# Optimization experiments

Hardware: AMD Instinct MI355X
Metric: run time of the kernel (lower is better)

Reference implementation:

```python
import jax, jax.numpy as jnp
import numpy as np

N_USERS = 100000
N_ITEMS = 20000
N_GENRES = 20
N_TAGS = 1128
EMB_ID = 64
EMB_FEAT = 64
HEADS = 8
HIDDEN = 256
D_MOVIE = EMB_ID + 2 * EMB_FEAT  # 192
E_HALF = 200000
N_NODES = N_USERS + N_ITEMS
NEG_SLOPE = 0.2


def setup_inputs() -> dict:
    key = jax.random.key(0)
    ks = jax.random.split(key, 24)
    p = lambda k, shape: (jax.random.normal(k, shape, jnp.float32) * 0.05)
    user_ids = jnp.arange(N_USERS)
    movie_ids = jnp.arange(N_ITEMS)
    mov_x = jax.random.normal(ks[0], (N_ITEMS, N_GENRES + N_TAGS), jnp.float32)
    # bipartite user<->movie edges, both directions (no self loops, matches add_self_loops=False)
    u = jax.random.randint(ks[1], (E_HALF,), 0, N_USERS)
    m = jax.random.randint(ks[2], (E_HALF,), 0, N_ITEMS) + N_USERS
    edge_index = jnp.stack([jnp.concatenate([u, m]), jnp.concatenate([m, u])])  # [2, 2*E_HALF]
    C1 = HIDDEN // HEADS
    return dict(
        user_ids=user_ids, movie_ids=movie_ids, mov_x=mov_x, edge_index=edge_index,
        user_emb=p(ks[3], (N_USERS, EMB_ID)), item_emb=p(ks[4], (N_ITEMS, EMB_ID)),
        gW1=p(ks[5], (N_GENRES, EMB_FEAT)), gb1=jnp.zeros((EMB_FEAT,), jnp.float32),
        gW2=p(ks[6], (EMB_FEAT, EMB_FEAT)), gb2=jnp.zeros((EMB_FEAT,), jnp.float32),
        tW1=p(ks[7], (N_TAGS, EMB_FEAT)), tb1=jnp.zeros((EMB_FEAT,), jnp.float32),
        tW2=p(ks[8], (EMB_FEAT, EMB_FEAT)), tb2=jnp.zeros((EMB_FEAT,), jnp.float32),
        Ws1=p(ks[9], (D_MOVIE, HIDDEN)), Wd1=p(ks[10], (D_MOVIE, HIDDEN)),
        as1=p(ks[11], (HEADS, C1)), ad1=p(ks[12], (HEADS, C1)),
        b1=jnp.zeros((HIDDEN,), jnp.float32),
        Ws2=p(ks[13], (HIDDEN, HIDDEN)), Wd2=p(ks[14], (HIDDEN, HIDDEN)),
        as2=p(ks[15], (1, HIDDEN)), ad2=p(ks[16], (1, HIDDEN)),
        b2=jnp.zeros((HIDDEN,), jnp.float32),
    )


def _gat(x, edge_index, Ws, Wd, a_s, a_d, bias, concat):
    # PyG GATConv (eval mode: dropout off, add_self_loops=False)
    N = x.shape[0]
    H, C = a_s.shape
    hs = (x @ Ws).reshape(N, H, C)  # source-side projection
    hd = (x @ Wd).reshape(N, H, C)  # dest-side projection
    al_s = (hs * a_s).sum(-1)  # [N, H]
    al_d = (hd * a_d).sum(-1)  # [N, H]
    src, dst = edge_index[0], edge_index[1]
    e = al_s[src] + al_d[dst]                      # [E, H]
    e = jnp.where(e > 0, e, NEG_SLOPE * e)         # leaky_relu(0.2)
    mmax = jax.ops.segment_max(e, dst, num_segments=N)
    w = jnp.exp(e - mmax[dst])
    ssum = jax.ops.segment_sum(w, dst, num_segments=N)
    alpha = w / (ssum[dst] + 1e-16)                # segment softmax over incoming edges
    out = jax.ops.segment_sum(hs[src] * alpha[:, :, None], dst, num_segments=N)  # [N, H, C]
    out = out.reshape(N, H * C) if concat else out.mean(axis=1)
    return out + bias


def reference(user_ids, movie_ids, mov_x, edge_index,
              user_emb, item_emb,
              gW1, gb1, gW2, gb2, tW1, tb1, tW2, tb2,
              Ws1, Wd1, as1, ad1, b1,
              Ws2, Wd2, as2, ad2, b2):
    g_feat = mov_x[:, :N_GENRES]
    t_feat = mov_x[:, N_GENRES:]
    g = jax.nn.relu(g_feat @ gW1 + gb1) @ gW2 + gb2
    t = jax.nn.relu(t_feat @ tW1 + tb1) @ tW2 + tb2
    x_mov = jnp.concatenate([item_emb[movie_ids], g, t], axis=1)  # [n_m, D_MOVIE]
    # homogeneous graph: user nodes first (zero-pad user emb to D_MOVIE), then movies
    x_usr = jnp.pad(user_emb[user_ids], ((0, 0), (0, D_MOVIE - EMB_ID)))
    x = jnp.concatenate([x_usr, x_mov], axis=0)  # [N_NODES, D_MOVIE]
    out = jax.nn.elu(_gat(x, edge_index, Ws1, Wd1, as1, ad1, b1, concat=True))
    out = _gat(out, edge_index, Ws2, Wd2, as2, ad2, b2, concat=False)
    ptr = jnp.array([0, N_USERS, N_USERS + N_ITEMS])
    return out, ptr
```

## Files before the change

### kernel.cpp

```cpp
#include <hip/hip_runtime.h>
#include <hip/hip_bf16.h>

#define N_USERS_C 100000
#define N_ITEMS_C 20000
#define N_NODES_C 120000
#define E_TOT_C   400000
#define D_IN_C    192
#define HID_C     256
#define NEG_C     0.2f
#define CLAMP_C   1000.0f
#define KPAD_C    1152
#define NB_SCAN   ((N_NODES_C + 255) / 256)
#define NB_EDGE   ((E_TOT_C + 255) / 256)
#define NB_GEMM   (N_NODES_C / 64)
#define NB_G1U    1562
#define NB_G1M    (NB_GEMM - NB_G1U)
#define ROWE      40
#define NT_MOV    313
#define KSPLIT    4
#define KCH       288
#define NSTEP_MOV (KCH / 32)

typedef __attribute__((ext_vector_type(8))) short bfrag;
typedef __attribute__((ext_vector_type(4))) float ffrag;

__device__ __forceinline__ float bf2f(unsigned short u){
  return __uint_as_float(((unsigned)u) << 16);
}
__device__ __forceinline__ float ldf(const void* p, long i, int isf32){
  return isf32 ? ((const float*)p)[i] : bf2f(((const unsigned short*)p)[i]);
}
__device__ __forceinline__ float sane(float v){
  return (v > -1e30f && v < 1e30f) ? v : 0.f;
}
__device__ __forceinline__ int clampsrc(int s){
  return s < 0 ? 0 : (s >= N_NODES_C ? N_NODES_C - 1 : s);
}
__device__ __forceinline__ short f2bs(float f){
  __hip_bfloat16 h = __float2bfloat16(f);
  return *reinterpret_cast<short*>(&h);
}

__global__ __launch_bounds__(256) void detect_dtype(const unsigned short* __restrict__ ue,
                                                    int* __restrict__ flag){
  __shared__ int cnt[256];
  int tid = threadIdx.x; int c = 0;
  for (int i = tid; i < 8192; i += 256){
    unsigned e = (ue[i] >> 7) & 0xFFu;
    if (e >= 129u) c++;
  }
  cnt[tid] = c; __syncthreads();
  if (tid == 0){
    int s = 0;
    for (int i = 0; i < 256; i++) s += cnt[i];
    *flag = (s > 100) ? 1 : 0;
  }
}

struct PrepArgs {
  const void *ue, *ie;
  const void *gW1, *gb1, *gW2, *gb2, *tW1, *tb1, *tW2, *tb2;
  const void *Ws1, *Wd1, *as1, *ad1, *b1, *Ws2, *Wd2, *as2, *ad2, *b2;
  __hip_bfloat16 *x, *Bt1, *Bt2, *W1t, *W2t, *b1c, *b2c, *bg1, *bg2;
  int *deg, *cursor;
  const int* flag;
};

#define NB_UEMB  3125
#define NB_UZERO 2
#define NB_MOVE  625
#define NB_BT1   204
#define NB_BT2   272
#define NB_W1T   72
#define NB_W2T   8
#define NB_ZERO  235
#define NB_PREP (NB_UEMB+NB_UZERO+NB_MOVE+NB_BT1+NB_BT2+NB_W1T+NB_W2T+1+NB_ZERO)

__global__ __launch_bounds__(256) void mega_prep(PrepArgs a){
  int b = blockIdx.x, tid = threadIdx.x;
  int f32 = *a.flag;
  if (b < NB_UEMB) {
    int idx = b * 256 + tid;
    int n = idx >> 3, c0 = (idx & 7) * 8;
    union { short s[8]; float4 f; } u;
    if (f32) {
      const float* rf = (const float*)a.ue + (long)n * 64 + c0;
      float4 x0 = *(const float4*)rf, x1 = *(const float4*)(rf + 4);
      u.s[0]=f2bs(x0.x); u.s[1]=f2bs(x0.y); u.s[2]=f2bs(x0.z); u.s[3]=f2bs(x0.w);
      u.s[4]=f2bs(x1.x); u.s[5]=f2bs(x1.y); u.s[6]=f2bs(x1.z); u.s[7]=f2bs(x1.w);
    } else {
      u.f = *(const float4*)((const unsigned short*)a.ue + (long)n * 64 + c0);
    }
    *(float4*)(&a.x[(long)n * 192 + c0]) = u.f;
    return;
  }
  b -= NB_UEMB;
  if (b < NB_UZERO) {
    int idx = b * 256 + tid;
    int r = idx >> 4, c0 = 64 + (idx & 15) * 8;
    float4 z = {0.f, 0.f, 0.f, 0.f};
    *(float4*)(&a.x[(long)(99968 + r) * 192 + c0]) = z;
    return;
  }
  b -= NB_UZERO;
  if (b < NB_MOVE) {
    int idx = b * 256 + tid;
    int m = idx >> 3, c0 = (idx & 7) * 8;
    union { short s[8]; float4 f; } u;
    if (f32) {
      const float* rf = (const float*)a.ie + (long)m * 64 + c0;
      float4 x0 = *(const float4*)rf, x1 = *(const float4*)(rf + 4);
      u.s[0]=f2bs(x0.x); u.s[1]=f2bs(x0.y); u.s[2]=f2bs(x0.z); u.s[3]=f2bs(x0.w);
      u.s[4]=f2bs(x1.x); u.s[5]=f2bs(x1.y); u.s[6]=f2bs(x1.z); u.s[7]=f2bs(x1.w);
    } else {
      u.f = *(const float4*)((const unsigned short*)a.ie + (long)m * 64 + c0);
    }
    *(float4*)(&a.x[(long)(N_USERS_C + m) * 192 + c0]) = u.f;
    return;
  }
  b -= NB_MOVE;
  if (b < NB_BT1) {
    int idx = b * 256 + tid;
    int col = idx / 192, k = idx - col * 192;
    float v;
    if (col < 256) v = ldf(a.Ws1, k * 256 + col, f32);
    else if (col < 264) {
      int h = col - 256; float s = 0.f;
      for (int c = 0; c < 32; c++)
        s += ldf(a.Ws1, k * 256 + h * 32 + c, f32) * ldf(a.as1, h * 32 + c, f32);
      v = s;
    } else {
      int h = col - 264; float s = 0.f;
      for (int c = 0; c < 32; c++)
        s += ldf(a.Wd1, k * 256 + h * 32 + c, f32) * ldf(a.ad1, h * 32 + c, f32);
      v = s;
    }
    a.Bt1[col * 192 + k] = __float2bfloat16(v);
    return;
  }
  b -= NB_BT1;
  if (b < NB_BT2) {
    int idx = b * 256 + tid;
    int col = idx / 256, k = idx & 255;
    float v;
    if (col < 256) v = ldf(a.Ws2, k * 256 + col, f32);
    else if (col == 256) {
      float s = 0.f;
      for (int c = 0; c < 256; c++)
        s += ldf(a.Ws2, k * 256 + c, f32) * ldf(a.as2, c, f32);
      v = s;
    } else if (col == 257) {
      float s = 0.f;
      for (int c = 0; c < 256; c++)
        s += ldf(a.Wd2, k * 256 + c, f32) * ldf(a.ad2, c, f32);
      v = s;
    } else v = 0.f;
    a.Bt2[col * 256 + k] = __float2bfloat16(v);
    return;
  }
  b -= NB_BT2;
  if (b < NB_W1T) {
    int idx = b * 256 + tid;
    int n = idx / 144, c8 = idx - n * 144;
    int k0 = c8 * 8;
    union { short s[8]; float4 f; } u;
#pragma unroll
    for (int j = 0; j < 8; j++) {
      int k = k0 + j; float v = 0.f;
      if (n < 64) { if (k < 20) v = ldf(a.gW1, k * 64 + n, f32); }
      else        { if (k >= 20 && k < 1148) v = ldf(a.tW1, (k - 20) * 64 + (n - 64), f32); }
      u.s[j] = f2bs(v);
    }
    *(float4*)(&a.W1t[(long)n * 1152 + k0]) = u.f;
    return;
  }
  b -= NB_W1T;
  if (b < NB_W2T) {
    int idx = b * 256 + tid;
    int n = idx >> 4, k0 = (idx & 15) * 8;
    union { short s[8]; float4 f; } u;
#pragma unroll
    for (int j = 0; j < 8; j++) {
      int k = k0 + j; float v = 0.f;
      if (n < 64) { if (k < 64)  v = ldf(a.gW2, k * 64 + n, f32); }
      else        { if (k >= 64) v = ldf(a.tW2, (k - 64) * 64 + (n - 64), f32); }
      u.s[j] = f2bs(v);
    }
    *(float4*)(&a.W2t[n * 128 + k0]) = u.f;
    return;
  }
  b -= NB_W2T;
  if (b < 1) {
    int i = tid;
    if (i < 64)       a.b1c[i] = __float2bfloat16(ldf(a.gb1, i, f32));
    else if (i < 128) a.b1c[i] = __float2bfloat16(ldf(a.tb1, i - 64, f32));
    else if (i < 192) a.b2c[i - 128] = __float2bfloat16(ldf(a.gb2, i - 128, f32));
    else              a.b2c[i - 128] = __float2bfloat16(ldf(a.tb2, i - 192, f32));
    a.bg1[tid] = __float2bfloat16(ldf(a.b1, tid, f32));
    a.bg2[tid] = __float2bfloat16(ldf(a.b2, tid, f32));
    return;
  }
  b -= 1;
  {
    int i0 = (b * 256 + tid) * 4;
    if (i0 < 2 * N_NODES_C) {
      int4 z = {0, 0, 0, 0};
      if (i0 < N_NODES_C) *(int4*)(a.deg + i0) = z;
      else                *(int4*)(a.cursor + (i0 - N_NODES_C)) = z;
    }
  }
}


__device__ void movie_k_body(int bid, const void* __restrict__ rawA, int f32v,
                             const __hip_bfloat16* __restrict__ W1t,
                             float* __restrict__ part,
                             short* __restrict__ Bls, short* __restrict__ Als){
  int tid = threadIdx.x;
  int wave = tid >> 6, lane = tid & 63, l15 = lane & 15, quad = lane >> 4;
  int tile = bid % NT_MOV, split = bid / NT_MOV;
  int rowbase_blk = tile * 64;
  int rowbase = rowbase_blk + wave * 16;
  ffrag acc[8];
#pragma unroll
  for (int i = 0; i < 8; i++) acc[i] = (ffrag){0.f, 0.f, 0.f, 0.f};
  const short* Bs = (const short*)W1t;
  int sr = tid >> 2, sc = tid & 3;
  int arow_st = rowbase_blk + sr; if (arow_st >= N_ITEMS_C) arow_st = N_ITEMS_C - 1;
  int r0 = tid >> 2, r1 = r0 + 64, cb = (tid & 3) * 8;
  int kbeg = split * KCH;

  auto loadA = [&](int k0) -> float4 {
    int kc = k0 + sc * 8;
    union { short s[8]; float4 f; } u;
    long base = (long)arow_st * 1148 + kc;
    if (kc + 8 <= 1148) {
      if (f32v) {
        const float* rf = (const float*)rawA + base;
        float4 x0 = *(const float4*)rf, x1 = *(const float4*)(rf + 4);
        u.s[0]=f2bs(x0.x); u.s[1]=f2bs(x0.y); u.s[2]=f2bs(x0.z); u.s[3]=f2bs(x0.w);
        u.s[4]=f2bs(x1.x); u.s[5]=f2bs(x1.y); u.s[6]=f2bs(x1.z); u.s[7]=f2bs(x1.w);
      } else {
        const unsigned short* rs = (const unsigned short*)rawA + base;
        ushort4 a0 = *(const ushort4*)rs, a1 = *(const ushort4*)(rs + 4);
        u.s[0]=(short)a0.x; u.s[1]=(short)a0.y; u.s[2]=(short)a0.z; u.s[3]=(short)a0.w;
        u.s[4]=(short)a1.x; u.s[5]=(short)a1.y; u.s[6]=(short)a1.z; u.s[7]=(short)a1.w;
      }
    } else {
#pragma unroll
      for (int j = 0; j < 8; j++) {
        float v = (kc + j < 1148) ? ldf(rawA, base + j, f32v) : 0.f;
        u.s[j] = f2bs(v);
      }
    }
    return u.f;
  };

  float4 aR = loadA(kbeg);
  float4 bR0 = *(const float4*)(Bs + (long)r0 * KPAD_C + kbeg + cb);
  float4 bR1 = *(const float4*)(Bs + (long)r1 * KPAD_C + kbeg + cb);

  for (int s = 0; s < NSTEP_MOV; s++) {
    *(float4*)(&Als[sr * ROWE + sc * 8]) = aR;
    *(float4*)(&Bls[r0 * ROWE + cb]) = bR0;
    *(float4*)(&Bls[r1 * ROWE + cb]) = bR1;
    __syncthreads();
    if (s + 1 < NSTEP_MOV) {
      int kn = kbeg + (s + 1) * 32;
      aR = loadA(kn);
      bR0 = *(const float4*)(Bs + (long)r0 * KPAD_C + kn + cb);
      bR1 = *(const float4*)(Bs + (long)r1 * KPAD_C + kn + cb);
    }
    int koff = quad * 8;
    bfrag af = *(const bfrag*)(&Als[(wave * 16 + l15) * ROWE + koff]);
#pragma unroll
    for (int nt = 0; nt < 8; nt++) {
      bfrag bf = *(const bfrag*)(&Bls[(nt * 16 + l15) * ROWE + koff]);
      acc[nt] = __builtin_amdgcn_mfma_f32_16x16x32_bf16(af, bf, acc[nt], 0, 0, 0);
    }
    __syncthreads();
  }
  float* pb = part + (long)split * (N_ITEMS_C * 128);
#pragma unroll
  for (int reg = 0; reg < 4; reg++) {
    int grow = rowbase + quad * 4 + reg;
    if (grow >= N_ITEMS_C) continue;
#pragma unroll
    for (int nt = 0; nt < 8; nt++)
      pb[(long)grow * 128 + nt * 16 + l15] = acc[nt][reg];
  }
}

__device__ void movie2_body(int bid, const float* __restrict__ part,
                            const __hip_bfloat16* __restrict__ b1c,
                            const __hip_bfloat16* __restrict__ W2t,
                            const __hip_bfloat16* __restrict__ b2c,
                            __hip_bfloat16* __restrict__ out,
                            short* __restrict__ Bls, short* __restrict__ Als){
  int tid = threadIdx.x;
  int wave = tid >> 6, lane = tid & 63, l15 = lane & 15, quad = lane >> 4;
  int rowbase_blk = bid * 64;
  int rowbase = rowbase_blk + wave * 16;
  ffrag acc[8];
#pragma unroll
  for (int i = 0; i < 8; i++) acc[i] = (ffrag){0.f, 0.f, 0.f, 0.f};
  const short* Bs = (const short*)W2t;
  int sr = tid >> 2, sc = tid & 3;
  int arow_st = rowbase_blk + sr; if (arow_st >= N_ITEMS_C) arow_st = N_ITEMS_C - 1;
  for (int k0 = 0; k0 < 128; k0 += 32) {
    __syncthreads();
    for (int t = tid; t < 512; t += 256) {
      int r = t >> 2, c = t & 3;
      *(float4*)(&Bls[r * ROWE + c * 8]) =
          *(const float4*)(Bs + (long)r * 128 + k0 + c * 8);
    }
    int kc = k0 + sc * 8;
    float vs[8];
#pragma unroll
    for (int j = 0; j < 8; j++) vs[j] = __bfloat162float(b1c[kc + j]);
    long base = (long)arow_st * 128 + kc;
#pragma unroll
    for (int s = 0; s < KSPLIT; s++) {
      const float* p = part + (long)s * (N_ITEMS_C * 128) + base;
      float4 q0 = *(const float4*)p, q1 = *(const float4*)(p + 4);
      vs[0] += q0.x; vs[1] += q0.y; vs[2] += q0.z; vs[3] += q0.w;
      vs[4] += q1.x; vs[5] += q1.y; vs[6] += q1.z; vs[7] += q1.w;
    }
    union { short s[8]; float4 f; } u;
#pragma unroll
    for (int j = 0; j < 8; j++) u.s[j] = f2bs(fmaxf(vs[j], 0.f));
    *(float4*)(&Als[sr * ROWE + sc * 8]) = u.f;
    __syncthreads();
    int koff = quad * 8;
    bfrag af = *(const bfrag*)(&Als[(wave * 16 + l15) * ROWE + koff]);
#pragma unroll
    for (int nt = 0; nt < 8; nt++) {
      bfrag bf = *(const bfrag*)(&Bls[(nt * 16 + l15) * ROWE + koff]);
      acc[nt] = __builtin_amdgcn_mfma_f32_16x16x32_bf16(af, bf, acc[nt], 0, 0, 0);
    }
  }
#pragma unroll
  for (int reg = 0; reg < 4; reg++) {
    int grow = rowbase + quad * 4 + reg;
    if (grow >= N_ITEMS_C) continue;
#pragma unroll
    for (int nt = 0; nt < 8; nt++) {
      float v = acc[nt][reg] + __bfloat162float(b2c[nt * 16 + l15]);
      out[(long)grow * D_IN_C + 64 + nt * 16 + l15] = __float2bfloat16(v);
    }
  }
}

__device__ void gemm_fused_body(int bid,
    const __hip_bfloat16* __restrict__ A, const __hip_bfloat16* __restrict__ Bt,
    __hip_bfloat16* __restrict__ Hout, float* __restrict__ als, float* __restrict__ ald,
    int K, int natt, int ukmax,
    short* __restrict__ Bls, short* __restrict__ Als){
  int tid = threadIdx.x;
  int wave = tid >> 6, lane = tid & 63, l15 = lane & 15, quad = lane >> 4;
  int rowbase_blk = bid * 64;
  int rowbase = rowbase_blk + wave * 16;
  int kmax = (rowbase_blk + 64 <= N_USERS_C) ? ukmax : K;
  ffrag acc[17];
#pragma unroll
  for (int i = 0; i < 17; i++) acc[i] = (ffrag){0.f, 0.f, 0.f, 0.f};
  const short* As = (const short*)A;
  const short* Bs = (const short*)Bt;
  int sr = tid >> 2, sc = tid & 3;
  long arow = (long)(rowbase_blk + sr) * K;
  float4 aR = *(const float4*)(As + arow + sc * 8);
  for (int k0 = 0; k0 < kmax; k0 += 32) {
    *(float4*)(&Als[sr * ROWE + sc * 8]) = aR;
    for (int t = tid; t < 1088; t += 256) {
      int r = t >> 2, c = t & 3;
      *(float4*)(&Bls[r * ROWE + c * 8]) = *(const float4*)(Bs + (long)r * K + k0 + c * 8);
    }
    __syncthreads();
    if (k0 + 32 < kmax)
      aR = *(const float4*)(As + arow + k0 + 32 + sc * 8);
    int koff = quad * 8;
    bfrag af = *(const bfrag*)(&Als[(wave * 16 + l15) * ROWE + koff]);
#pragma unroll
    for (int nt = 0; nt < 17; nt++) {
      bfrag bf = *(const bfrag*)(&Bls[(nt * 16 + l15) * ROWE + koff]);
      acc[nt] = __builtin_amdgcn_mfma_f32_16x16x32_bf16(af, bf, acc[nt], 0, 0, 0);
    }
    __syncthreads();
  }
  int col = l15;
#pragma unroll
  for (int reg = 0; reg < 4; reg++) {
    int grow = rowbase + quad * 4 + reg;
    long obase = (long)grow * 256;
#pragma unroll
    for (int nt = 0; nt < 16; nt++)
      Hout[obase + nt * 16 + col] = __float2bfloat16(acc[nt][reg]);
    float v = acc[16][reg];
    if (col < natt) als[grow * natt + col] = v;
    else if (col < 2 * natt) ald[grow * natt + (col - natt)] = v;
  }
}

__device__ void deg_count_body(int e, const int* __restrict__ ei, int* __restrict__ deg){
  if (e >= E_TOT_C) return;
  int dst = ei[E_TOT_C + e];
  if (dst >= 0 && dst < N_NODES_C) atomicAdd(&deg[dst], 1);
}

__device__ void deg_bsum_body(int bid, const int* __restrict__ deg, int* __restrict__ bsum){
  int i = bid * 256 + threadIdx.x;
  int v = (i < N_NODES_C) ? deg[i] : 0;
#pragma unroll
  for (int o = 32; o > 0; o >>= 1) v += __shfl_down(v, o, 64);
  __shared__ int ws[4];
  int wave = threadIdx.x >> 6, lane = threadIdx.x & 63;
  if (lane == 0) ws[wave] = v;
  __syncthreads();
  if (threadIdx.x == 0) bsum[bid] = ws[0] + ws[1] + ws[2] + ws[3];
}

__device__ void scatter_body(int e, const int* __restrict__ ei, const int* __restrict__ ptrn,
                             int* __restrict__ cursor, int* __restrict__ elist_src){
  if (e >= E_TOT_C) return;
  int dst = ei[E_TOT_C + e];
  if (dst < 0 || dst >= N_NODES_C) return;
  int pos = atomicAdd(&cursor[dst], 1);
  elist_src[ptrn[dst] + pos] = ei[e];
}

#define NB_BIG (NT_MOV * KSPLIT + NB_G1U + NB_EDGE)
__global__ __launch_bounds__(256) void fused_stage3(
    const void* __restrict__ rawA, const int* __restrict__ flag,
    const __hip_bfloat16* __restrict__ W1t, float* __restrict__ part,
    const __hip_bfloat16* __restrict__ x, const __hip_bfloat16* __restrict__ Bt1,
    __hip_bfloat16* __restrict__ hs, float* __restrict__ als, float* __restrict__ ald,
    const int* __restrict__ ei, int* __restrict__ deg){
  __shared__ short smem[(272 + 64) * ROWE];
  int b = blockIdx.x;
  if (b < NT_MOV * KSPLIT)
    movie_k_body(b, rawA, *flag, W1t, part, smem, smem + 128 * ROWE);
  else if (b < NT_MOV * KSPLIT + NB_G1U)
    gemm_fused_body(b - NT_MOV * KSPLIT, x, Bt1, hs, als, ald, 192, 8, 64,
                    smem, smem + 272 * ROWE);
  else
    deg_count_body((b - NT_MOV * KSPLIT - NB_G1U) * 256 + threadIdx.x, ei, deg);
}

#define NB_KB (NT_MOV + NB_SCAN)
__global__ __launch_bounds__(256) void movie2_bsum(
    const float* __restrict__ part, const __hip_bfloat16* __restrict__ b1c,
    const __hip_bfloat16* __restrict__ W2t, const __hip_bfloat16* __restrict__ b2c,
    __hip_bfloat16* __restrict__ out,
    const int* __restrict__ deg, int* __restrict__ bsum){
  __shared__ short smem[192 * ROWE];
  int b = blockIdx.x;
  if (b < NT_MOV) movie2_body(b, part, b1c, W2t, b2c, out, smem, smem + 128 * ROWE);
  else deg_bsum_body(b - NT_MOV, deg, bsum);
}

#define NB_S7 (NB_G1M + NB_EDGE)
__global__ __launch_bounds__(256) void gemm1mov_scatter(
    const __hip_bfloat16* __restrict__ A, const __hip_bfloat16* __restrict__ Bt,
    __hip_bfloat16* __restrict__ Hout, float* __restrict__ als, float* __restrict__ ald,
    const int* __restrict__ ei, const int* __restrict__ ptrn,
    int* __restrict__ cursor, int* __restrict__ elist_src){
  __shared__ short smem[(272 + 64) * ROWE];
  int b = blockIdx.x;
  if (b < NB_G1M)
    gemm_fused_body(NB_G1U + b, A, Bt, Hout, als, ald, 192, 8, 64,
                    smem, smem + 272 * ROWE);
  else
    scatter_body((b - NB_G1M) * 256 + threadIdx.x, ei, ptrn, cursor, elist_src);
}

__global__ __launch_bounds__(256) void gemm_fused(
    const __hip_bfloat16* __restrict__ A, const __hip_bfloat16* __restrict__ Bt,
    __hip_bfloat16* __restrict__ Hout, float* __restrict__ als, float* __restrict__ ald,
    int K, int natt, int ukmax){
  __shared__ short smem[(272 + 64) * ROWE];
  gemm_fused_body(blockIdx.x, A, Bt, Hout, als, ald, K, natt, ukmax,
                  smem, smem + 272 * ROWE);
}

__global__ __launch_bounds__(512) void bsum_scan(int* __restrict__ bsum,
                                                 int* __restrict__ ptrn){
  __shared__ int sm[512];
  int t = threadIdx.x;
  int v = (t < NB_SCAN) ? bsum[t] : 0;
  sm[t] = v;
  __syncthreads();
  for (int o = 1; o < 512; o <<= 1) {
    int add = (t >= o) ? sm[t - o] : 0;
    __syncthreads();
    sm[t] += add;
    __syncthreads();
  }
  int excl = (t == 0) ? 0 : sm[t - 1];
  if (t < NB_SCAN) bsum[t] = excl;
  if (t == NB_SCAN - 1) ptrn[N_NODES_C] = sm[t];
}

__global__ __launch_bounds__(256) void deg_scan_final(const int* __restrict__ deg,
                                                      const int* __restrict__ bexcl,
                                                      int* __restrict__ ptrn){
  __shared__ int sm[256];
  int i = blockIdx.x * 256 + threadIdx.x;
  int t = threadIdx.x;
  int v = (i < N_NODES_C) ? deg[i] : 0;
  sm[t] = v;
  __syncthreads();
  for (int o = 1; o < 256; o <<= 1) {
    int add = (t >= o) ? sm[t - o] : 0;
    __syncthreads();
    sm[t] += add;
    __syncthreads();
  }
  int excl = (t == 0) ? 0 : sm[t - 1];
  if (i < N_NODES_C) ptrn[i] = bexcl[blockIdx.x] + excl;
}

__global__ __launch_bounds__(256) void aggregate1(
    const int* __restrict__ ptrn, const int* __restrict__ elist_src,
    const float* __restrict__ als, const float* __restrict__ ald,
    const __hip_bfloat16* __restrict__ hs, const __hip_bfloat16* __restrict__ bias,
    __hip_bfloat16* __restrict__ h1){
  int node = blockIdx.x * 4 + (threadIdx.x >> 6);
  if (node >= N_NODES_C) return;
  int lane = threadIdx.x & 63;
  int c0 = lane * 4;
  int h = lane >> 3;
  int beg = ptrn[node], end = ptrn[node + 1];
  float aldv = sane(ald[node * 8 + h]);
  float m = -1e30f;
  float wsum = 0.f, a0 = 0.f, a1 = 0.f, a2 = 0.f, a3 = 0.f;
  const unsigned short* hsu = (const unsigned short*)hs;
  float alsv_p = 0.f;
  ushort4 hv_p = {0, 0, 0, 0};
  int src_b = 0;
  if (beg < end) {
    int s0 = clampsrc(elist_src[beg]);
    alsv_p = als[(long)s0 * 8 + h];
    hv_p = *(const ushort4*)(hsu + (long)s0 * 256 + c0);
    if (beg + 1 < end) src_b = clampsrc(elist_src[beg + 1]);
  }
  for (int i = beg; i < end; i++) {
    float alsv = alsv_p;
    ushort4 hv = hv_p;
    if (i + 1 < end) {
      alsv_p = als[(long)src_b * 8 + h];
      hv_p = *(const ushort4*)(hsu + (long)src_b * 256 + c0);
    }
    if (i + 2 < end)
      src_b = clampsrc(elist_src[i + 2]);
    float ev = sane(alsv) + aldv;
    ev = ev > 0.f ? ev : NEG_C * ev;
    float mnew = fmaxf(m, ev);
    float corr = __expf(m - mnew);
    float w = __expf(ev - mnew);
    m = mnew;
    wsum = wsum * corr + w;
    a0 = a0 * corr + w * bf2f(hv.x); a1 = a1 * corr + w * bf2f(hv.y);
    a2 = a2 * corr + w * bf2f(hv.z); a3 = a3 * corr + w * bf2f(hv.w);
  }
  float inv = 1.f / (wsum + 1e-16f);
  float v0 = a0 * inv + __bfloat162float(bias[c0 + 0]);
  float v1 = a1 * inv + __bfloat162float(bias[c0 + 1]);
  float v2 = a2 * inv + __bfloat162float(bias[c0 + 2]);
  float v3 = a3 * inv + __bfloat162float(bias[c0 + 3]);
  v0 = v0 > 0.f ? v0 : (__expf(v0) - 1.f);
  v1 = v1 > 0.f ? v1 : (__expf(v1) - 1.f);
  v2 = v2 > 0.f ? v2 : (__expf(v2) - 1.f);
  v3 = v3 > 0.f ? v3 : (__expf(v3) - 1.f);
  v0 = fminf(fmaxf(v0, -CLAMP_C), CLAMP_C);
  v1 = fminf(fmaxf(v1, -CLAMP_C), CLAMP_C);
  v2 = fminf(fmaxf(v2, -CLAMP_C), CLAMP_C);
  v3 = fminf(fmaxf(v3, -CLAMP_C), CLAMP_C);
  long ob = (long)node * 256 + c0;
  h1[ob + 0] = __float2bfloat16(v0); h1[ob + 1] = __float2bfloat16(v1);
  h1[ob + 2] = __float2bfloat16(v2); h1[ob + 3] = __float2bfloat16(v3);
}

__global__ __launch_bounds__(256) void aggregate2(
    const int* __restrict__ ptrn, const int* __restrict__ elist_src,
    const float* __restrict__ als, const float* __restrict__ ald,
    const __hip_bfloat16* __restrict__ hs, const __hip_bfloat16* __restrict__ bias,
    float* __restrict__ out, int out_size){
  if (blockIdx.x == 0 && threadIdx.x == 0) {
    out[out_size - 3] = 0.f;
    out[out_size - 2] = (float)N_USERS_C;
    out[out_size - 1] = (float)N_NODES_C;
  }
  int node = blockIdx.x * 4 + (threadIdx.x >> 6);
  if (node >= N_NODES_C) return;
  int lane = threadIdx.x & 63;
  int c0 = lane * 4;
  int beg = ptrn[node], end = ptrn[node + 1];
  float aldv = sane(ald[node]);
  float m = -1e30f;
  float wsum = 0.f, a0 = 0.f, a1 = 0.f, a2 = 0.f, a3 = 0.f;
  const unsigned short* hsu = (const unsigned short*)hs;
  float alsv_p = 0.f;
  ushort4 hv_p = {0, 0, 0, 0};
  int src_b = 0;
  if (beg < end) {
    int s0 = clampsrc(elist_src[beg]);
    alsv_p = als[s0];
    hv_p = *(const ushort4*)(hsu + (long)s0 * 256 + c0);
    if (beg + 1 < end) src_b = clampsrc(elist_src[beg + 1]);
  }
  for (int i = beg; i < end; i++) {
    float alsv = alsv_p;
    ushort4 hv = hv_p;
    if (i + 1 < end) {
      alsv_p = als[src_b];
      hv_p = *(const ushort4*)(hsu + (long)src_b * 256 + c0);
    }
    if (i + 2 < end)
      src_b = clampsrc(elist_src[i + 2]);
    float ev = sane(alsv) + aldv;
    ev = ev > 0.f ? ev : NEG_C * ev;
    float mnew = fmaxf(m, ev);
    float corr = __expf(m - mnew);
    float w = __expf(ev - mnew);
    m = mnew;
    wsum = wsum * corr + w;
    a0 = a0 * corr + w * bf2f(hv.x); a1 = a1 * corr + w * bf2f(hv.y);
    a2 = a2 * corr + w * bf2f(hv.z); a3 = a3 * corr + w * bf2f(hv.w);
  }
  float inv = 1.f / (wsum + 1e-16f);
  float4 v;
  v.x = a0 * inv + __bfloat162float(bias[c0 + 0]);
  v.y = a1 * inv + __bfloat162float(bias[c0 + 1]);
  v.z = a2 * inv + __bfloat162float(bias[c0 + 2]);
  v.w = a3 * inv + __bfloat162float(bias[c0 + 3]);
  v.x = fminf(fmaxf(v.x, -CLAMP_C), CLAMP_C);
  v.y = fminf(fmaxf(v.y, -CLAMP_C), CLAMP_C);
  v.z = fminf(fmaxf(v.z, -CLAMP_C), CLAMP_C);
  v.w = fminf(fmaxf(v.w, -CLAMP_C), CLAMP_C);
  *(float4*)(out + (long)node * 256 + c0) = v;
}

extern "C" void kernel_launch(void* const* d_in, const int* in_sizes, int n_in,
                              void* d_out, int out_size, void* d_ws, size_t ws_size,
                              hipStream_t stream) {
  const void* mov_x    = d_in[2];
  const int*  ei       = (const int*)d_in[3];
  const void* user_emb = d_in[4];
  const void* item_emb = d_in[5];

  char* ws = (char*)d_ws;
  size_t off = 0;
  auto alloc = [&](size_t bytes) -> void* {
    void* p = ws + off; off += (bytes + 255) / 256 * 256; return p;
  };
  int* flag   = (int*)alloc(4);
  __hip_bfloat16* Bt1 = (__hip_bfloat16*)alloc(272 * 192 * 2);
  __hip_bfloat16* Bt2 = (__hip_bfloat16*)alloc(272 * 256 * 2);
  __hip_bfloat16* W1t = (__hip_bfloat16*)alloc(128 * KPAD_C * 2);
  __hip_bfloat16* W2t = (__hip_bfloat16*)alloc(128 * 128 * 2);
  __hip_bfloat16* b1c = (__hip_bfloat16*)alloc(128 * 2);
  __hip_bfloat16* b2c = (__hip_bfloat16*)alloc(128 * 2);
  __hip_bfloat16* bg1 = (__hip_bfloat16*)alloc(256 * 2);
  __hip_bfloat16* bg2 = (__hip_bfloat16*)alloc(256 * 2);
  int* ptrn   = (int*)alloc((N_NODES_C + 1) * 4);
  int* deg    = (int*)alloc(N_NODES_C * 4);
  int* cursor = (int*)alloc(N_NODES_C * 4);
  int* bsum   = (int*)alloc(512 * 4);
  int* elist  = (int*)alloc(E_TOT_C * 4);
  float* als  = (float*)alloc((size_t)N_NODES_C * 8 * 4);
  float* ald  = (float*)alloc((size_t)N_NODES_C * 8 * 4);
  float* part = (float*)alloc((size_t)KSPLIT * N_ITEMS_C * 128 * 4);
  __hip_bfloat16* x  = (__hip_bfloat16*)alloc((size_t)N_NODES_C * D_IN_C * 2);
  __hip_bfloat16* hs = (__hip_bfloat16*)alloc((size_t)N_NODES_C * HID_C * 2);
  __hip_bfloat16* h1  = (__hip_bfloat16*)d_out;

  detect_dtype<<<1, 256, 0, stream>>>((const unsigned short*)user_emb, flag);

  PrepArgs pa;
  pa.ue = user_emb; pa.ie = item_emb;
  pa.gW1 = d_in[6];  pa.gb1 = d_in[7];  pa.gW2 = d_in[8];  pa.gb2 = d_in[9];
  pa.tW1 = d_in[10]; pa.tb1 = d_in[11]; pa.tW2 = d_in[12]; pa.tb2 = d_in[13];
  pa.Ws1 = d_in[14]; pa.Wd1 = d_in[15]; pa.as1 = d_in[16]; pa.ad1 = d_in[17]; pa.b1 = d_in[18];
  pa.Ws2 = d_in[19]; pa.Wd2 = d_in[20]; pa.as2 = d_in[21]; pa.ad2 = d_in[22]; pa.b2 = d_in[23];
  pa.x = x; pa.Bt1 = Bt1; pa.Bt2 = Bt2; pa.W1t = W1t; pa.W2t = W2t;
  pa.b1c = b1c; pa.b2c = b2c; pa.bg1 = bg1; pa.bg2 = bg2;
  pa.deg = deg; pa.cursor = cursor; pa.flag = flag;
  mega_prep<<<NB_PREP, 256, 0, stream>>>(pa);

  fused_stage3<<<NB_BIG, 256, 0, stream>>>(mov_x, flag, W1t, part,
                                           x, Bt1, hs, als, ald, ei, deg);
  movie2_bsum<<<NB_KB, 256, 0, stream>>>(part, b1c, W2t, b2c,
                                         x + (long)N_USERS_C * D_IN_C, deg, bsum);
  bsum_scan<<<1, 512, 0, stream>>>(bsum, ptrn);
  deg_scan_final<<<NB_SCAN, 256, 0, stream>>>(deg, bsum, ptrn);

  gemm1mov_scatter<<<NB_S7, 256, 0, stream>>>(x, Bt1, hs, als, ald,
                                              ei, ptrn, cursor, elist);
  aggregate1<<<N_NODES_C / 4, 256, 0, stream>>>(ptrn, elist, als, ald, hs, bg1, h1);

  gemm_fused<<<NB_GEMM, 256, 0, stream>>>(h1, Bt2, hs, als, ald, 256, 1, 256);
  aggregate2<<<N_NODES_C / 4, 256, 0, stream>>>(ptrn, elist, als, ald, hs, bg2,
                                                (float*)d_out, out_size);
}
```

Measured before the change: 558.7 us.

## Interleave heterogeneous block roles in fused kernels to balance scheduling

Block indices in three fused multi-role kernels are remapped so that the different kinds of work (movie GEMM K-split, user GEMM, degree counting, scan partial sums, scatter) are interleaved instead of laid out in contiguous ranges. The aim is to mix compute-heavy and memory-bound blocks on the CUs at the same time, so long-running GEMM blocks are not all queued first and short atomic blocks do not finish separately at the end. The mappings rely on hardcoded block counts (3756, 310, 785, 313*6), which silently break if the constants change.

```diff
diff --git a/kernel.cpp b/kernel.cpp
--- a/kernel.cpp
+++ b/kernel.cpp
@@ -437,16 +437,20 @@
     const int* __restrict__ ei, int* __restrict__ deg){
   __shared__ short smem[(272 + 64) * ROWE];
   int b = blockIdx.x;
-  if (b < NT_MOV * KSPLIT)
-    movie_k_body(b, rawA, *flag, W1t, part, smem, smem + 128 * ROWE);
-  else if (b < NT_MOV * KSPLIT + NB_G1U)
-    gemm_fused_body(b - NT_MOV * KSPLIT, x, Bt1, hs, als, ald, 192, 8, 64,
+  int role, idx;
+  if (b < 3756) { role = b % 3; idx = b / 3; }
+  else { int t = b - 3756; if (t < 310) { role = 1; idx = 1252 + t; }
+         else { role = 2; idx = 1252 + (t - 310); } }
+  if (role == 0)
+    movie_k_body(idx, rawA, *flag, W1t, part, smem, smem + 128 * ROWE);
+  else if (role == 1)
+    gemm_fused_body(idx, x, Bt1, hs, als, ald, 192, 8, 64,
                     smem, smem + 272 * ROWE);
   else
-    deg_count_body((b - NT_MOV * KSPLIT - NB_G1U) * 256 + threadIdx.x, ei, deg);
-}
-
-#define NB_KB (NT_MOV + NB_SCAN)
+    deg_count_body(idx * 256 + threadIdx.x, ei, deg);
+}
+
+#define NB_KB 785
 __global__ __launch_bounds__(256) void movie2_bsum(
     const float* __restrict__ part, const __hip_bfloat16* __restrict__ b1c,
     const __hip_bfloat16* __restrict__ W2t, const __hip_bfloat16* __restrict__ b2c,
@@ -454,11 +458,17 @@
     const int* __restrict__ deg, int* __restrict__ bsum){
   __shared__ short smem[192 * ROWE];
   int b = blockIdx.x;
-  if (b < NT_MOV) movie2_body(b, part, b1c, W2t, b2c, out, smem, smem + 128 * ROWE);
-  else deg_bsum_body(b - NT_MOV, deg, bsum);
-}
-
-#define NB_S7 (NB_G1M + NB_EDGE)
+  int c = b / 5, r = b % 5;
+  if (r < 2) {
+    int idx = c * 2 + r;
+    if (idx < NT_MOV) movie2_body(idx, part, b1c, W2t, b2c, out, smem, smem + 128 * ROWE);
+  } else {
+    int idx = c * 3 + (r - 2);
+    if (idx < NB_SCAN) deg_bsum_body(idx, deg, bsum);
+  }
+}
+
+#define NB_S7 (313 * 6)
 __global__ __launch_bounds__(256) void gemm1mov_scatter(
     const __hip_bfloat16* __restrict__ A, const __hip_bfloat16* __restrict__ Bt,
     __hip_bfloat16* __restrict__ Hout, float* __restrict__ als, float* __restrict__ ald,
@@ -466,11 +476,15 @@
     int* __restrict__ cursor, int* __restrict__ elist_src){
   __shared__ short smem[(272 + 64) * ROWE];
   int b = blockIdx.x;
-  if (b < NB_G1M)
-    gemm_fused_body(NB_G1U + b, A, Bt, Hout, als, ald, 192, 8, 64,
-                    smem, smem + 272 * ROWE);
-  else
-    scatter_body((b - NB_G1M) * 256 + threadIdx.x, ei, ptrn, cursor, elist_src);
+  int c = b / 6, r = b % 6;
+  if (r == 0) {
+    if (c < NB_G1M)
+      gemm_fused_body(NB_G1U + c, A, Bt, Hout, als, ald, 192, 8, 64,
+                      smem, smem + 272 * ROWE);
+  } else {
+    int idx = c * 5 + (r - 1);
+    scatter_body(idx * 256 + threadIdx.x, ei, ptrn, cursor, elist_src);
+  }
 }
 
 __global__ __launch_bounds__(256) void gemm_fused(
```

After: 560.6 us. No clear change (+0.3%).
